# Optimization experiments

Measured on AMD Instinct MI355X. Metric: run time of the kernel, lower is better.

The kernel has to match this reference:

```python
import jax, jax.numpy as jnp
import numpy as np

B, N, DIM, K = 4, 4096, 128, 16


def setup_inputs() -> dict:
    key = jax.random.key(0)
    ks = jax.random.split(key, 20)
    s = 0.05
    inp = {
        "x": jax.random.normal(ks[0], (B, N, DIM), jnp.float32),
        "pos": jax.random.normal(ks[1], (B, N, 3), jnp.float32),
        # pos_mlp: Linear(3,dim) -> ReLU -> Linear(dim,dim)
        "pw1": jax.random.normal(ks[2], (3, DIM), jnp.float32) * s,
        "pb1": jnp.zeros((DIM,), jnp.float32),
        "pw2": jax.random.normal(ks[3], (DIM, DIM), jnp.float32) * s,
        "pb2": jnp.zeros((DIM,), jnp.float32),
        # q/k/v projections
        "qw": jax.random.normal(ks[4], (DIM, DIM), jnp.float32) * s,
        "qb": jnp.zeros((DIM,), jnp.float32),
        "kw": jax.random.normal(ks[5], (DIM, DIM), jnp.float32) * s,
        "kb": jnp.zeros((DIM,), jnp.float32),
        "vw": jax.random.normal(ks[6], (DIM, DIM), jnp.float32) * s,
        "vb": jnp.zeros((DIM,), jnp.float32),
        # attn MLP: Linear(dim, dim//4) -> ReLU -> Linear(dim//4, dim)
        "aw1": jax.random.normal(ks[7], (DIM, DIM // 4), jnp.float32) * s,
        "ab1": jnp.zeros((DIM // 4,), jnp.float32),
        "aw2": jax.random.normal(ks[8], (DIM // 4, DIM), jnp.float32) * s,
        "ab2": jnp.zeros((DIM,), jnp.float32),
    }
    return inp


def reference(x, pos, pw1, pb1, pw2, pb2, qw, qb, kw, kb, vw, vb, aw1, ab1, aw2, ab2):
    Bs, Np, C = x.shape
    k = K
    # pairwise squared distances: |pi|^2 + |pj|^2 - 2 pi.pj  -> (B,N,N)
    inner = jnp.einsum('bnd,bmd->bnm', pos, pos)
    xx = jnp.sum(pos * pos, axis=2, keepdims=True)  # (B,N,1)
    dist = xx + jnp.swapaxes(xx, 1, 2) - 2.0 * inner
    # k nearest neighbors (smallest dist) -> indices (B,N,k)
    _, idx = jax.lax.top_k(-dist, k)
    bidx = jnp.arange(Bs)[:, None, None]
    neighbors = x[bidx, idx]        # (B,N,k,C)
    pos_neighbors = pos[bidx, idx]  # (B,N,k,3)
    pos_relative = pos[:, :, None, :] - pos_neighbors  # (B,N,k,3)
    # pos MLP
    pe = jax.nn.relu(pos_relative @ pw1 + pb1) @ pw2 + pb2  # (B,N,k,C)
    q = (x @ qw + qb)[:, :, None, :]   # (B,N,1,C)
    kk = neighbors @ kw + kb           # (B,N,k,C)
    v = neighbors @ vw + vb            # (B,N,k,C)
    a = q - kk + pe
    attn = jax.nn.relu(a @ aw1 + ab1) @ aw2 + ab2  # (B,N,k,C)
    attn = jax.nn.softmax(attn, axis=2)
    out = jnp.sum(attn * (v + pe), axis=2)  # (B,N,C)
    return out
```

## Files before the change

### kernel.cpp

```cpp
#include <hip/hip_runtime.h>
#include <hip/hip_bf16.h>
#include <stdint.h>

#define BATCH 4
#define NPTS  4096
#define DIM   128
#define KNN   16
#define NROWS (BATCH*NPTS)
#define NCHUNK 16
#define CHUNK  (NPTS/NCHUNK)

typedef unsigned long long u64;
typedef unsigned int u32;
typedef unsigned short u16;
typedef __attribute__((ext_vector_type(8))) short short8;
typedef __attribute__((ext_vector_type(4))) float f32x4;

__device__ __forceinline__ u16 f2bf(float f) {
  u32 u = __float_as_uint(f);
  u += 0x7FFFu + ((u >> 16) & 1);
  return (u16)(u >> 16);
}

__global__ __launch_bounds__(256) void prep_pos4(const float* __restrict__ pos,
                                                 float4* __restrict__ pos4) {
  int i = blockIdx.x * 256 + threadIdx.x;
  if (i < NROWS) pos4[i] = make_float4(pos[3*i], pos[3*i+1], pos[3*i+2], 0.f);
}

__global__ __launch_bounds__(256) void prep_matmul(
    const float* __restrict__ pw2, const float* __restrict__ qw, const float* __restrict__ kw,
    const float* __restrict__ aw1,
    u16* __restrict__ w1T, float* __restrict__ Wq2, float* __restrict__ Wk2) {
  int p = blockIdx.x >> 2, qtr = blockIdx.x & 3;
  const float* A = p == 0 ? pw2 : (p == 1 ? qw : kw);
  int j = threadIdx.x & 31;
  int r0 = qtr*32 + (threadIdx.x >> 5)*4;
  float acc[4] = {0.f,0.f,0.f,0.f};
  for (int c = 0; c < 128; ++c) {
    float av = aw1[c*32 + j];
#pragma unroll
    for (int rr = 0; rr < 4; ++rr) acc[rr] = fmaf(A[(r0+rr)*128 + c], av, acc[rr]);
  }
#pragma unroll
  for (int rr = 0; rr < 4; ++rr) {
    int h = r0 + rr;
    if (p == 0)      w1T[j*128 + (h ^ ((j&7)<<3))] = f2bf(acc[rr]);
    else if (p == 1) Wq2[h*32 + j] = acc[rr];
    else             Wk2[h*32 + j] = acc[rr];
  }
}

__global__ __launch_bounds__(256) void prep_convert(
    const float* __restrict__ pw2, const float* __restrict__ aw2,
    const float* __restrict__ pw1, const float* __restrict__ pb1,
    const float* __restrict__ qb, const float* __restrict__ kb,
    const float* __restrict__ pb2, const float* __restrict__ aw1, const float* __restrict__ ab1,
    u16* __restrict__ pw2T, u16* __restrict__ aw2T,
    float4* __restrict__ pw1q, float* __restrict__ bias1) {
  int bid = blockIdx.x, tid = threadIdx.x;
  if (bid < 64) {
    int e = bid*256 + tid; int k = e >> 7, n = e & 127;
    pw2T[n*128 + (k ^ ((n&7)<<3))] = f2bf(pw2[k*128 + n]);
  } else if (bid < 80) {
    int e = (bid-64)*256 + tid; int k = e >> 7, n = e & 127;
    aw2T[n*32 + (k ^ ((n&3)<<3))] = f2bf(aw2[k*128 + n]);
  } else {
    if (tid < 128) {
      int c = tid;
      pw1q[c ^ ((c & 0x18) >> 2)] = make_float4(pw1[c], pw1[128+c], pw1[256+c], pb1[c]);
    } else if (tid < 160) {
      int j = tid - 128;
      float s = ab1[j];
      for (int c = 0; c < 128; ++c) s += (qb[c]-kb[c]+pb2[c]) * aw1[c*32+j];
      bias1[j] = s;
    }
  }
}

template <typename T>
__device__ __forceinline__ void cex(T& a, T& b) {
  T mn = a < b ? a : b;
  T mx = a < b ? b : a;
  a = mn; b = mx;
}
template <typename T>
__device__ __forceinline__ void sort16(T x[16]) {
#pragma unroll
  for (int k = 2; k <= 16; k <<= 1)
#pragma unroll
    for (int j = k >> 1; j > 0; j >>= 1)
#pragma unroll
      for (int i = 0; i < 16; ++i) {
        int l = i ^ j;
        if (l > i) { if ((i & k) == 0) cex(x[i], x[l]); else cex(x[l], x[i]); }
      }
}
template <typename T>
__device__ __forceinline__ void merge16(T A[16], const T B[16]) {
#pragma unroll
  for (int i = 0; i < 16; ++i) { T b = B[15 - i]; A[i] = A[i] < b ? A[i] : b; }
#pragma unroll
  for (int j = 8; j > 0; j >>= 1)
#pragma unroll
    for (int i = 0; i < 16; ++i) { int l = i ^ j; if (l > i) cex(A[i], A[l]); }
}
__device__ __forceinline__ void bmerge32(u32 x[32]) {
#pragma unroll
  for (int j = 16; j > 0; j >>= 1)
#pragma unroll
    for (int i = 0; i < 32; ++i) { int l = i ^ j; if (l > i) cex(x[i], x[l]); }
}

__global__ __launch_bounds__(256) void knn_scan(const float4* __restrict__ pos4,
                                                u32* __restrict__ part) {
  __shared__ float4 cs[4][CHUNK];
  const int lane  = threadIdx.x & 63;
  const int w     = threadIdx.x >> 6;
  const int task  = blockIdx.x * 4 + w;
  const int qg    = task >> 4;
  const int chunk = task & 15;
  const int qbase = qg * 64;
  const int b     = qbase >> 12;
  const int cbase = chunk * CHUNK;

  const float4* cand = pos4 + b*NPTS + cbase;
#pragma unroll
  for (int i = 0; i < CHUNK/64; ++i) cs[w][lane + 64*i] = cand[lane + 64*i];
  __syncthreads();

  float4 qp = pos4[qbase + lane];
  const float qx = qp.x, qy = qp.y, qz = qp.z;

  u32 best[16];
#pragma unroll
  for (int i = 0; i < 16; ++i) best[i] = ~0u;

#pragma unroll 1
  for (int m = 0; m < CHUNK/16; ++m) {
    u32 batch[16];
#pragma unroll
    for (int e = 0; e < 16; ++e) {
      float4 p = cs[w][m*16 + e];
      float dx = qx - p.x, dy = qy - p.y, dz = qz - p.z;
      float d  = fmaf(dx, dx, fmaf(dy, dy, dz*dz));
      batch[e] = (__float_as_uint(d) & 0xFFFFF000u) | (u32)(cbase + m*16 + e);
    }
    sort16(batch);
    merge16(best, batch);
  }
  const int q = qbase + lane;
  uint4* dst = (uint4*)(part + q*256 + chunk*16);
#pragma unroll
  for (int t = 0; t < 4; ++t)
    dst[t] = make_uint4(best[4*t], best[4*t+1], best[4*t+2], best[4*t+3]);
}

__global__ __launch_bounds__(256) void knn_refine(const float4* __restrict__ pos4,
                                                  const u32* __restrict__ part,
                                                  int* __restrict__ knnIdx) {
  __shared__ u64 A64[16][137];
  __shared__ u32 Bu[16][264];
  u32 (*Au)[274] = (u32 (*)[274])A64;

  const int tid = threadIdx.x;
  const int qi = tid >> 4, c = tid & 15;
  const int q  = blockIdx.x * 16 + qi;
  const int b  = q >> 12;

  {
    const uint4* src = (const uint4*)(part + q*256 + c*16);
    u32 own[16];
#pragma unroll
    for (int t = 0; t < 4; ++t) {
      uint4 v = src[t];
      own[4*t+0]=v.x; own[4*t+1]=v.y; own[4*t+2]=v.z; own[4*t+3]=v.w;
    }
#pragma unroll
    for (int s = 0; s < 16; ++s) Au[qi][c*17 + s] = own[s];
  }
  __syncthreads();

  if (c < 8) {
    u32 x[32];
#pragma unroll
    for (int s = 0; s < 16; ++s) x[s]      = Au[qi][(2*c)*17 + s];
#pragma unroll
    for (int s = 0; s < 16; ++s) x[16 + s] = Au[qi][(2*c+1)*17 + 15 - s];
    bmerge32(x);
#pragma unroll
    for (int s = 0; s < 32; ++s) Bu[qi][c*33 + s] = x[s];
  }
  __syncthreads();

  if (c < 4) {
    u32 x[32];
#pragma unroll
    for (int s = 0; s < 32; ++s) {
      u32 a = Bu[qi][(2*c)*33 + s], bb = Bu[qi][(2*c+1)*33 + 31 - s];
      x[s] = a < bb ? a : bb;
    }
    bmerge32(x);
#pragma unroll
    for (int s = 0; s < 32; ++s) Au[qi][c*33 + s] = x[s];
  }
  __syncthreads();

  if (c < 2) {
    u32 x[32];
#pragma unroll
    for (int s = 0; s < 32; ++s) {
      u32 a = Au[qi][(2*c)*33 + s], bb = Au[qi][(2*c+1)*33 + 31 - s];
      x[s] = a < bb ? a : bb;
    }
    bmerge32(x);
#pragma unroll
    for (int s = 0; s < 32; ++s) Bu[qi][c*33 + s] = x[s];
  }
  __syncthreads();

  if (c == 0) {
    u32 x[32];
#pragma unroll
    for (int s = 0; s < 32; ++s) {
      u32 a = Bu[qi][s], bb = Bu[qi][33 + 31 - s];
      x[s] = a < bb ? a : bb;
    }
    bmerge32(x);
#pragma unroll
    for (int s = 0; s < 32; ++s) Bu[qi][132 + s] = x[s];
  }
  __syncthreads();

  if (c < 2) {
    float4 qp = pos4[q];
    const double qx = qp.x, qy = qp.y, qz = qp.z;
    u64 key[16];
#pragma unroll
    for (int s = 0; s < 16; ++s) {
      int idx = (int)(Bu[qi][132 + c*16 + s] & 0xFFFu);
      float4 p = pos4[(b<<12) + idx];
      double dx = qx - (double)p.x;
      double dy = qy - (double)p.y;
      double dz = qz - (double)p.z;
      double d  = fma(dx, dx, fma(dy, dy, dz*dz));
      key[s] = (((u64)__double_as_longlong(d)) & ~0xFFFull) | (u64)idx;
    }
    sort16(key);
#pragma unroll
    for (int s = 0; s < 16; ++s) A64[qi][c*17 + s] = key[s];
  }
  __syncthreads();

  if (c == 0) {
    u64 best[16], nb[16];
#pragma unroll
    for (int s = 0; s < 16; ++s) { best[s] = A64[qi][s]; nb[s] = A64[qi][17 + s]; }
    merge16(best, nb);
    const int outq = q * KNN;
#pragma unroll
    for (int s = 0; s < 16; ++s) knnIdx[outq + s] = (int)(best[s] & 0xFFFull);
  }
}

__global__ __launch_bounds__(256) void proj_v(
    const float* __restrict__ x,
    const float* __restrict__ vw, const float* __restrict__ vb,
    const float* __restrict__ Wq2, const float* __restrict__ Wk2,
    float* __restrict__ vo, float* __restrict__ qa, float* __restrict__ ka) {
  __shared__ float xs[32*DIM];
  const int row0 = blockIdx.x * 32;
  const int tid = threadIdx.x;
  {
    const float4* src = (const float4*)(x + row0*DIM);
    float4* dst = (float4*)xs;
#pragma unroll
    for (int i = 0; i < 4; ++i) dst[tid + 256*i] = src[tid + 256*i];
  }
  __syncthreads();
  {
    const int c = tid & 127, g2 = tid >> 7;
    float av[16];
#pragma unroll
    for (int r = 0; r < 16; ++r) av[r] = 0.f;
    for (int d4 = 0; d4 < 32; ++d4) {
      float wv[4];
#pragma unroll
      for (int t = 0; t < 4; ++t) wv[t] = vw[(d4*4+t)*DIM + c];
#pragma unroll
      for (int r = 0; r < 16; ++r) {
        float4 xv = *(const float4*)&xs[(g2*16+r)*DIM + d4*4];
        av[r] = fmaf(xv.x, wv[0], av[r]);
        av[r] = fmaf(xv.y, wv[1], av[r]);
        av[r] = fmaf(xv.z, wv[2], av[r]);
        av[r] = fmaf(xv.w, wv[3], av[r]);
      }
    }
    float bv = vb[c];
#pragma unroll
    for (int r = 0; r < 16; ++r) vo[(row0 + g2*16 + r)*DIM + c] = av[r] + bv;
  }
  {
    const int j = tid & 31, grp = tid >> 5;
    float aq[4] = {0.f,0.f,0.f,0.f}, ak[4] = {0.f,0.f,0.f,0.f};
    for (int d4 = 0; d4 < 32; ++d4) {
#pragma unroll
      for (int t = 0; t < 4; ++t) {
        int d = d4*4 + t;
        float wq = Wq2[d*32 + j], wk = Wk2[d*32 + j];
#pragma unroll
        for (int rr = 0; rr < 4; ++rr) {
          float xv = xs[(grp*4+rr)*DIM + d];
          aq[rr] = fmaf(xv, wq, aq[rr]);
          ak[rr] = fmaf(xv, wk, ak[rr]);
        }
      }
    }
#pragma unroll
    for (int rr = 0; rr < 4; ++rr) {
      qa[(row0 + grp*4 + rr)*32 + j] = aq[rr];
      ka[(row0 + grp*4 + rr)*32 + j] = ak[rr];
    }
  }
}

__global__ __launch_bounds__(256) void attn_mfma(
    const float4* __restrict__ pos4, const int* __restrict__ knnIdx,
    const float* __restrict__ vws, const float* __restrict__ qa, const float* __restrict__ ka,
    const u16* __restrict__ pw2T, const u16* __restrict__ w1T, const u16* __restrict__ aw2T,
    const float4* __restrict__ pw1q, const float* __restrict__ bias1,
    const float* __restrict__ pb2, const float* __restrict__ ab2,
    float* __restrict__ out) {
  __shared__ __align__(16) u16 pw2s[16384];
  __shared__ __align__(16) u16 w1s[4096];
  __shared__ __align__(16) u16 aw2s[4096];
  __shared__ __align__(16) float4 pw1s[128];
  __shared__ float bias1s[32];
  __shared__ float pb2s[128];
  __shared__ float ab2s[128];
  __shared__ __align__(16) u16 h2t[4][512];
  __shared__ float4 rels[4][16];
  __shared__ int ids[4][16];

  const int tid = threadIdx.x;
  {
    const uint4* s1 = (const uint4*)pw2T; uint4* d1 = (uint4*)pw2s;
#pragma unroll
    for (int i = 0; i < 8; ++i) d1[tid + 256*i] = s1[tid + 256*i];
    const uint4* s2 = (const uint4*)w1T; uint4* d2 = (uint4*)w1s;
#pragma unroll
    for (int i = 0; i < 2; ++i) d2[tid + 256*i] = s2[tid + 256*i];
    const uint4* s3 = (const uint4*)aw2T; uint4* d3 = (uint4*)aw2s;
#pragma unroll
    for (int i = 0; i < 2; ++i) d3[tid + 256*i] = s3[tid + 256*i];
    if (tid < 128) { pw1s[tid] = pw1q[tid]; pb2s[tid] = pb2[tid]; ab2s[tid] = ab2[tid]; }
    else if (tid < 160) bias1s[tid-128] = bias1[tid-128];
  }
  __syncthreads();

  const int lane = tid & 63, w = tid >> 6;
  const int c16 = lane & 15, g = lane >> 4;

  for (int it = 0; it < 4; ++it) {
    const int q = blockIdx.x*16 + w*4 + it;
    const int b = q >> 12;
    if (lane < 16) {
      int id = knnIdx[q*KNN + lane];
      ids[w][lane] = id;
      float4 pq = pos4[q], pn = pos4[(b<<12) + id];
      rels[w][lane] = make_float4(pq.x-pn.x, pq.y-pn.y, pq.z-pn.z, 0.f);
    }
    __syncthreads();

    int idr[4];
#pragma unroll
    for (int r = 0; r < 4; ++r) idr[r] = ids[w][g*4 + r];

    float qa_v[2], ka_v[2][4];
#pragma unroll
    for (int t = 0; t < 2; ++t) qa_v[t] = qa[q*32 + t*16 + c16];
#pragma unroll
    for (int r = 0; r < 4; ++r)
#pragma unroll
      for (int t = 0; t < 2; ++t) ka_v[t][r] = ka[((b<<12)+idr[r])*32 + t*16 + c16];

    float4 rl = rels[w][c16];
    short8 h1f[4];
#pragma unroll
    for (int kc = 0; kc < 4; ++kc) {
      short8 s;
#pragma unroll
      for (int j = 0; j < 8; ++j) {
        int c = kc*32 + g*8 + j;
        float4 wv = pw1s[c ^ ((c & 0x18) >> 2)];
        float h = fmaf(rl.x, wv.x, fmaf(rl.y, wv.y, fmaf(rl.z, wv.z, wv.w)));
        s[j] = (short)f2bf(fmaxf(h, 0.f));
      }
      h1f[kc] = s;
    }

    f32x4 pe[8];
#pragma unroll
    for (int nt = 0; nt < 8; ++nt) { f32x4 z = {0.f,0.f,0.f,0.f}; pe[nt] = z; }
#pragma unroll
    for (int kc = 0; kc < 4; ++kc)
#pragma unroll
      for (int nt = 0; nt < 8; ++nt) {
        int n = nt*16 + c16;
        short8 bf = *(const short8*)&pw2s[n*128 + ((kc*32 + g*8) ^ ((n&7)<<3))];
        pe[nt] = __builtin_amdgcn_mfma_f32_16x16x32_bf16(h1f[kc], bf, pe[nt], 0, 0, 0);
      }

    f32x4 ha[2];
#pragma unroll
    for (int t = 0; t < 2; ++t) { f32x4 z = {0.f,0.f,0.f,0.f}; ha[t] = z; }
#pragma unroll
    for (int kc = 0; kc < 4; ++kc)
#pragma unroll
      for (int t = 0; t < 2; ++t) {
        int n = t*16 + c16;
        short8 bf = *(const short8*)&w1s[n*128 + ((kc*32 + g*8) ^ ((n&7)<<3))];
        ha[t] = __builtin_amdgcn_mfma_f32_16x16x32_bf16(h1f[kc], bf, ha[t], 0, 0, 0);
      }

#pragma unroll
    for (int t = 0; t < 2; ++t)
#pragma unroll
      for (int r = 0; r < 4; ++r) {
        float v = ha[t][r] + qa_v[t] - ka_v[t][r] + bias1s[t*16 + c16];
        int row = g*4 + r, col = t*16 + c16;
        h2t[w][row*32 + (col ^ ((row&3)<<3))] = f2bf(fmaxf(v, 0.f));
      }
    __syncthreads();

    short8 h2f = *(const short8*)&h2t[w][c16*32 + ((g*8) ^ ((c16&3)<<3))];

    f32x4 lg[8];
#pragma unroll
    for (int nt = 0; nt < 8; ++nt) {
      int n = nt*16 + c16;
      float ab = ab2s[n];
      f32x4 cini = {ab, ab, ab, ab};
      short8 bf = *(const short8*)&aw2s[n*32 + ((g*8) ^ ((n&3)<<3))];
      lg[nt] = __builtin_amdgcn_mfma_f32_16x16x32_bf16(h2f, bf, cini, 0, 0, 0);
    }

    float vv[8][4];
#pragma unroll
    for (int r = 0; r < 4; ++r) {
      const float* vrow = vws + (size_t)((b<<12) + idr[r])*DIM;
#pragma unroll
      for (int nt = 0; nt < 8; ++nt) vv[nt][r] = vrow[nt*16 + c16];
    }

#pragma unroll
    for (int nt = 0; nt < 8; ++nt) {
      float m = fmaxf(fmaxf(lg[nt][0], lg[nt][1]), fmaxf(lg[nt][2], lg[nt][3]));
      m = fmaxf(m, __shfl_xor(m, 16));
      m = fmaxf(m, __shfl_xor(m, 32));
      float e0 = __expf(lg[nt][0]-m), e1 = __expf(lg[nt][1]-m),
            e2 = __expf(lg[nt][2]-m), e3 = __expf(lg[nt][3]-m);
      float s = e0+e1+e2+e3;
      s += __shfl_xor(s, 16);
      s += __shfl_xor(s, 32);
      float inv = 1.0f / s;
      float pb = pb2s[nt*16 + c16];
      float acc = e0*(vv[nt][0] + pe[nt][0] + pb)
                + e1*(vv[nt][1] + pe[nt][1] + pb)
                + e2*(vv[nt][2] + pe[nt][2] + pb)
                + e3*(vv[nt][3] + pe[nt][3] + pb);
      acc *= inv;
      acc += __shfl_xor(acc, 16);
      acc += __shfl_xor(acc, 32);
      if (lane < 16) out[q*DIM + nt*16 + lane] = acc;
    }
  }
}

extern "C" void kernel_launch(void* const* d_in, const int* in_sizes, int n_in,
                              void* d_out, int out_size, void* d_ws, size_t ws_size,
                              hipStream_t stream) {
  const float* x   = (const float*)d_in[0];
  const float* pos = (const float*)d_in[1];
  const float* pw1 = (const float*)d_in[2];
  const float* pb1 = (const float*)d_in[3];
  const float* pw2 = (const float*)d_in[4];
  const float* pb2 = (const float*)d_in[5];
  const float* qw  = (const float*)d_in[6];
  const float* qb  = (const float*)d_in[7];
  const float* kw  = (const float*)d_in[8];
  const float* kb  = (const float*)d_in[9];
  const float* vw  = (const float*)d_in[10];
  const float* vb  = (const float*)d_in[11];
  const float* aw1 = (const float*)d_in[12];
  const float* ab1 = (const float*)d_in[13];
  const float* aw2 = (const float*)d_in[14];
  const float* ab2 = (const float*)d_in[15];
  float* out = (float*)d_out;

  char* ws = (char*)d_ws;
  float4* pos4   = (float4*)(ws);
  int*    knnIdx = (int*)(ws + (1u<<20));
  u32*    part   = (u32*)(ws + (2u<<20));
  float*  vws    = (float*)(ws + (2u<<20));
  float*  qa     = (float*)(ws + (11u<<20));
  float*  ka     = (float*)(ws + (13u<<20));
  char*   wsw    = ws + (19u<<20);
  u16*    pw2T  = (u16*)(wsw);
  u16*    w1T   = (u16*)(wsw + 32768);
  u16*    aw2T  = (u16*)(wsw + 40960);
  float4* pw1q  = (float4*)(wsw + 49152);
  float*  bias1 = (float*)(wsw + 51200);
  float*  Wq2   = (float*)(wsw + 51328);
  float*  Wk2   = (float*)(wsw + 67712);

  prep_pos4<<<NROWS/256, 256, 0, stream>>>(pos, pos4);
  prep_matmul<<<12, 256, 0, stream>>>(pw2, qw, kw, aw1, w1T, Wq2, Wk2);
  prep_convert<<<81, 256, 0, stream>>>(pw2, aw2, pw1, pb1, qb, kb, pb2, aw1, ab1,
                                       pw2T, aw2T, pw1q, bias1);
  knn_scan<<<(NROWS/64)*NCHUNK/4, 256, 0, stream>>>(pos4, part);
  knn_refine<<<NROWS/16, 256, 0, stream>>>(pos4, part, knnIdx);
  proj_v<<<NROWS/32, 256, 0, stream>>>(x, vw, vb, Wq2, Wk2, vws, qa, ka);
  attn_mfma<<<NROWS/16, 256, 0, stream>>>(pos4, knnIdx, vws, qa, ka,
                                          pw2T, w1T, aw2T, pw1q, bias1, pb2, ab2, out);
}
```

Before: 251.8 us.

## Merge prep kernels, MFMA projections, kNN early-skip, register-resident attn weights

Folds the three prep kernels into one launch and adds bf16 transposed copies of vw, Wq2 and Wk2. The fp32 scalar projection kernel becomes a bf16 MFMA kernel. knn_scan skips the sort and merge of a batch when no lane has a candidate that beats its current worst neighbor. attn_mfma keeps the w1 and aw2 fragments in registers, exchanges neighbor ids and relative positions with shuffles instead of shared memory, replaces block barriers with a wave-level LDS wait, and swizzles block order. The projections lose precision through the bf16 conversion, and register pressure in the attention kernel rises.

```diff
diff --git a/kernel.cpp b/kernel.cpp
--- a/kernel.cpp
+++ b/kernel.cpp
@@ -22,50 +22,32 @@
   return (u16)(u >> 16);
 }
 
-__global__ __launch_bounds__(256) void prep_pos4(const float* __restrict__ pos,
-                                                 float4* __restrict__ pos4) {
-  int i = blockIdx.x * 256 + threadIdx.x;
-  if (i < NROWS) pos4[i] = make_float4(pos[3*i], pos[3*i+1], pos[3*i+2], 0.f);
-}
-
-__global__ __launch_bounds__(256) void prep_matmul(
-    const float* __restrict__ pw2, const float* __restrict__ qw, const float* __restrict__ kw,
-    const float* __restrict__ aw1,
-    u16* __restrict__ w1T, float* __restrict__ Wq2, float* __restrict__ Wk2) {
-  int p = blockIdx.x >> 2, qtr = blockIdx.x & 3;
-  const float* A = p == 0 ? pw2 : (p == 1 ? qw : kw);
-  int j = threadIdx.x & 31;
-  int r0 = qtr*32 + (threadIdx.x >> 5)*4;
-  float acc[4] = {0.f,0.f,0.f,0.f};
-  for (int c = 0; c < 128; ++c) {
-    float av = aw1[c*32 + j];
-#pragma unroll
-    for (int rr = 0; rr < 4; ++rr) acc[rr] = fmaf(A[(r0+rr)*128 + c], av, acc[rr]);
-  }
-#pragma unroll
-  for (int rr = 0; rr < 4; ++rr) {
-    int h = r0 + rr;
-    if (p == 0)      w1T[j*128 + (h ^ ((j&7)<<3))] = f2bf(acc[rr]);
-    else if (p == 1) Wq2[h*32 + j] = acc[rr];
-    else             Wk2[h*32 + j] = acc[rr];
-  }
-}
-
-__global__ __launch_bounds__(256) void prep_convert(
-    const float* __restrict__ pw2, const float* __restrict__ aw2,
+#define WAVE_LDS_FENCE() asm volatile("s_waitcnt lgkmcnt(0)" ::: "memory")
+
+__global__ __launch_bounds__(256) void prep_all(
+    const float* __restrict__ pos,
     const float* __restrict__ pw1, const float* __restrict__ pb1,
-    const float* __restrict__ qb, const float* __restrict__ kb,
-    const float* __restrict__ pb2, const float* __restrict__ aw1, const float* __restrict__ ab1,
-    u16* __restrict__ pw2T, u16* __restrict__ aw2T,
+    const float* __restrict__ pw2, const float* __restrict__ pb2,
+    const float* __restrict__ qw, const float* __restrict__ qb,
+    const float* __restrict__ kw, const float* __restrict__ kb,
+    const float* __restrict__ vw,
+    const float* __restrict__ aw1, const float* __restrict__ ab1,
+    const float* __restrict__ aw2,
+    float4* __restrict__ pos4, u16* __restrict__ pw2T, u16* __restrict__ aw2T,
+    u16* __restrict__ vwT, u16* __restrict__ w1T,
+    u16* __restrict__ Wq2T, u16* __restrict__ Wk2T,
     float4* __restrict__ pw1q, float* __restrict__ bias1) {
-  int bid = blockIdx.x, tid = threadIdx.x;
+  const int bid = blockIdx.x, tid = threadIdx.x;
   if (bid < 64) {
-    int e = bid*256 + tid; int k = e >> 7, n = e & 127;
+    int e = bid*256 + tid, k = e >> 7, n = e & 127;
     pw2T[n*128 + (k ^ ((n&7)<<3))] = f2bf(pw2[k*128 + n]);
   } else if (bid < 80) {
-    int e = (bid-64)*256 + tid; int k = e >> 7, n = e & 127;
+    int e = (bid-64)*256 + tid, k = e >> 7, n = e & 127;
     aw2T[n*32 + (k ^ ((n&3)<<3))] = f2bf(aw2[k*128 + n]);
-  } else {
+  } else if (bid < 144) {
+    int e = (bid-80)*256 + tid, k = e >> 7, n = e & 127;
+    vwT[n*128 + (k ^ ((n&7)<<3))] = f2bf(vw[k*128 + n]);
+  } else if (bid == 144) {
     if (tid < 128) {
       int c = tid;
       pw1q[c ^ ((c & 0x18) >> 2)] = make_float4(pw1[c], pw1[128+c], pw1[256+c], pb1[c]);
@@ -75,6 +57,27 @@
       for (int c = 0; c < 128; ++c) s += (qb[c]-kb[c]+pb2[c]) * aw1[c*32+j];
       bias1[j] = s;
     }
+  } else if (bid < 157) {
+    int p = (bid-145) >> 2, qtr = (bid-145) & 3;
+    const float* A = p == 0 ? pw2 : (p == 1 ? qw : kw);
+    int j = tid & 31, r0 = qtr*32 + (tid >> 5)*4;
+    float acc[4] = {0.f,0.f,0.f,0.f};
+    for (int c = 0; c < 128; ++c) {
+      float av = aw1[c*32 + j];
+#pragma unroll
+      for (int rr = 0; rr < 4; ++rr) acc[rr] = fmaf(A[(r0+rr)*128 + c], av, acc[rr]);
+    }
+#pragma unroll
+    for (int rr = 0; rr < 4; ++rr) {
+      int h = r0 + rr;
+      u16 v = f2bf(acc[rr]);
+      if (p == 0)      w1T [j*128 + (h ^ ((j&7)<<3))] = v;
+      else if (p == 1) Wq2T[j*128 + (h ^ ((j&7)<<3))] = v;
+      else             Wk2T[j*128 + (h ^ ((j&7)<<3))] = v;
+    }
+  } else {
+    int i = (bid-157)*256 + tid;
+    if (i < NROWS) pos4[i] = make_float4(pos[3*i], pos[3*i+1], pos[3*i+2], 0.f);
   }
 }
 
@@ -146,8 +149,13 @@
       float d  = fmaf(dx, dx, fmaf(dy, dy, dz*dz));
       batch[e] = (__float_as_uint(d) & 0xFFFFF000u) | (u32)(cbase + m*16 + e);
     }
-    sort16(batch);
-    merge16(best, batch);
+    u32 bmin = batch[0];
+#pragma unroll
+    for (int e = 1; e < 16; ++e) bmin = batch[e] < bmin ? batch[e] : bmin;
+    if (__any(bmin < best[15])) {
+      sort16(batch);
+      merge16(best, batch);
+    }
   }
   const int q = qbase + lane;
   uint4* dst = (uint4*)(part + q*256 + chunk*16);
@@ -263,68 +271,62 @@
   }
 }
 
-__global__ __launch_bounds__(256) void proj_v(
-    const float* __restrict__ x,
-    const float* __restrict__ vw, const float* __restrict__ vb,
-    const float* __restrict__ Wq2, const float* __restrict__ Wk2,
+__global__ __launch_bounds__(256) void proj_mfma(
+    const float* __restrict__ x, const u16* __restrict__ vwT,
+    const u16* __restrict__ Wq2T, const u16* __restrict__ Wk2T,
+    const float* __restrict__ vb,
     float* __restrict__ vo, float* __restrict__ qa, float* __restrict__ ka) {
-  __shared__ float xs[32*DIM];
-  const int row0 = blockIdx.x * 32;
-  const int tid = threadIdx.x;
-  {
-    const float4* src = (const float4*)(x + row0*DIM);
-    float4* dst = (float4*)xs;
-#pragma unroll
-    for (int i = 0; i < 4; ++i) dst[tid + 256*i] = src[tid + 256*i];
-  }
-  __syncthreads();
-  {
-    const int c = tid & 127, g2 = tid >> 7;
-    float av[16];
-#pragma unroll
-    for (int r = 0; r < 16; ++r) av[r] = 0.f;
-    for (int d4 = 0; d4 < 32; ++d4) {
-      float wv[4];
-#pragma unroll
-      for (int t = 0; t < 4; ++t) wv[t] = vw[(d4*4+t)*DIM + c];
-#pragma unroll
-      for (int r = 0; r < 16; ++r) {
-        float4 xv = *(const float4*)&xs[(g2*16+r)*DIM + d4*4];
-        av[r] = fmaf(xv.x, wv[0], av[r]);
-        av[r] = fmaf(xv.y, wv[1], av[r]);
-        av[r] = fmaf(xv.z, wv[2], av[r]);
-        av[r] = fmaf(xv.w, wv[3], av[r]);
-      }
-    }
-    float bv = vb[c];
-#pragma unroll
-    for (int r = 0; r < 16; ++r) vo[(row0 + g2*16 + r)*DIM + c] = av[r] + bv;
-  }
-  {
-    const int j = tid & 31, grp = tid >> 5;
-    float aq[4] = {0.f,0.f,0.f,0.f}, ak[4] = {0.f,0.f,0.f,0.f};
-    for (int d4 = 0; d4 < 32; ++d4) {
-#pragma unroll
-      for (int t = 0; t < 4; ++t) {
-        int d = d4*4 + t;
-        float wq = Wq2[d*32 + j], wk = Wk2[d*32 + j];
-#pragma unroll
-        for (int rr = 0; rr < 4; ++rr) {
-          float xv = xs[(grp*4+rr)*DIM + d];
-          aq[rr] = fmaf(xv, wq, aq[rr]);
-          ak[rr] = fmaf(xv, wk, ak[rr]);
-        }
-      }
-    }
-#pragma unroll
-    for (int rr = 0; rr < 4; ++rr) {
-      qa[(row0 + grp*4 + rr)*32 + j] = aq[rr];
-      ka[(row0 + grp*4 + rr)*32 + j] = ak[rr];
-    }
-  }
-}
-
-__global__ __launch_bounds__(256) void attn_mfma(
+  const int lane = threadIdx.x & 63, w = threadIdx.x >> 6;
+  const int c16 = lane & 15, g = lane >> 4;
+  const int row0 = (blockIdx.x*4 + w)*16;
+
+  const float* xrow = x + (size_t)(row0 + c16)*DIM;
+  short8 af[4];
+#pragma unroll
+  for (int kc = 0; kc < 4; ++kc) {
+    float4 a0 = *(const float4*)&xrow[kc*32 + g*8];
+    float4 a1 = *(const float4*)&xrow[kc*32 + g*8 + 4];
+    short8 s;
+    s[0]=(short)f2bf(a0.x); s[1]=(short)f2bf(a0.y); s[2]=(short)f2bf(a0.z); s[3]=(short)f2bf(a0.w);
+    s[4]=(short)f2bf(a1.x); s[5]=(short)f2bf(a1.y); s[6]=(short)f2bf(a1.z); s[7]=(short)f2bf(a1.w);
+    af[kc] = s;
+  }
+
+#pragma unroll
+  for (int nt = 0; nt < 8; ++nt) {
+    int n = nt*16 + c16;
+    float bb = vb[n];
+    f32x4 acc = {bb, bb, bb, bb};
+#pragma unroll
+    for (int kc = 0; kc < 4; ++kc) {
+      short8 bf = *(const short8*)&vwT[n*128 + ((kc*32 + g*8) ^ ((n&7)<<3))];
+      acc = __builtin_amdgcn_mfma_f32_16x16x32_bf16(af[kc], bf, acc, 0, 0, 0);
+    }
+#pragma unroll
+    for (int r = 0; r < 4; ++r)
+      vo[(size_t)(row0 + g*4 + r)*DIM + n] = acc[r];
+  }
+
+#pragma unroll
+  for (int t = 0; t < 2; ++t) {
+    int n = t*16 + c16;
+    f32x4 aq = {0.f,0.f,0.f,0.f}, ak = {0.f,0.f,0.f,0.f};
+#pragma unroll
+    for (int kc = 0; kc < 4; ++kc) {
+      short8 bq = *(const short8*)&Wq2T[n*128 + ((kc*32 + g*8) ^ ((n&7)<<3))];
+      short8 bk = *(const short8*)&Wk2T[n*128 + ((kc*32 + g*8) ^ ((n&7)<<3))];
+      aq = __builtin_amdgcn_mfma_f32_16x16x32_bf16(af[kc], bq, aq, 0, 0, 0);
+      ak = __builtin_amdgcn_mfma_f32_16x16x32_bf16(af[kc], bk, ak, 0, 0, 0);
+    }
+#pragma unroll
+    for (int r = 0; r < 4; ++r) {
+      qa[(row0 + g*4 + r)*32 + n] = aq[r];
+      ka[(row0 + g*4 + r)*32 + n] = ak[r];
+    }
+  }
+}
+
+__global__ __launch_bounds__(256, 4) void attn_mfma(
     const float4* __restrict__ pos4, const int* __restrict__ knnIdx,
     const float* __restrict__ vws, const float* __restrict__ qa, const float* __restrict__ ka,
     const u16* __restrict__ pw2T, const u16* __restrict__ w1T, const u16* __restrict__ aw2T,
@@ -332,27 +334,15 @@
     const float* __restrict__ pb2, const float* __restrict__ ab2,
     float* __restrict__ out) {
   __shared__ __align__(16) u16 pw2s[16384];
-  __shared__ __align__(16) u16 w1s[4096];
-  __shared__ __align__(16) u16 aw2s[4096];
   __shared__ __align__(16) float4 pw1s[128];
-  __shared__ float bias1s[32];
-  __shared__ float pb2s[128];
-  __shared__ float ab2s[128];
+  __shared__ float bias1s[32], pb2s[128], ab2s[128];
   __shared__ __align__(16) u16 h2t[4][512];
-  __shared__ float4 rels[4][16];
-  __shared__ int ids[4][16];
 
   const int tid = threadIdx.x;
   {
     const uint4* s1 = (const uint4*)pw2T; uint4* d1 = (uint4*)pw2s;
 #pragma unroll
     for (int i = 0; i < 8; ++i) d1[tid + 256*i] = s1[tid + 256*i];
-    const uint4* s2 = (const uint4*)w1T; uint4* d2 = (uint4*)w1s;
-#pragma unroll
-    for (int i = 0; i < 2; ++i) d2[tid + 256*i] = s2[tid + 256*i];
-    const uint4* s3 = (const uint4*)aw2T; uint4* d3 = (uint4*)aw2s;
-#pragma unroll
-    for (int i = 0; i < 2; ++i) d3[tid + 256*i] = s3[tid + 256*i];
     if (tid < 128) { pw1s[tid] = pw1q[tid]; pb2s[tid] = pb2[tid]; ab2s[tid] = ab2[tid]; }
     else if (tid < 160) bias1s[tid-128] = bias1[tid-128];
   }
@@ -361,20 +351,40 @@
   const int lane = tid & 63, w = tid >> 6;
   const int c16 = lane & 15, g = lane >> 4;
 
-  for (int it = 0; it < 4; ++it) {
-    const int q = blockIdx.x*16 + w*4 + it;
-    const int b = q >> 12;
-    if (lane < 16) {
-      int id = knnIdx[q*KNN + lane];
-      ids[w][lane] = id;
-      float4 pq = pos4[q], pn = pos4[(b<<12) + id];
-      rels[w][lane] = make_float4(pq.x-pn.x, pq.y-pn.y, pq.z-pn.z, 0.f);
-    }
-    __syncthreads();
-
+  short8 Bw1[4][2];
+#pragma unroll
+  for (int kc = 0; kc < 4; ++kc)
+#pragma unroll
+    for (int t = 0; t < 2; ++t) {
+      int n = t*16 + c16;
+      Bw1[kc][t] = *(const short8*)&w1T[n*128 + ((kc*32 + g*8) ^ ((n&7)<<3))];
+    }
+  short8 Baw2[8];
+#pragma unroll
+  for (int nt = 0; nt < 8; ++nt) {
+    int n = nt*16 + c16;
+    Baw2[nt] = *(const short8*)&aw2T[n*32 + ((g*8) ^ ((n&3)<<3))];
+  }
+
+  const int swz = (blockIdx.x & 7) * 128 + (blockIdx.x >> 3);
+  const int qblock = swz * 16;
+  const int qbase  = qblock + w * 4;
+  const int bofs   = (qblock >> 12) << 12;
+
+  int id_own = knnIdx[qbase*KNN + lane];
+  float4 pq = pos4[qbase + g];
+  float4 pn = pos4[bofs + id_own];
+  float rox = pq.x - pn.x, roy = pq.y - pn.y, roz = pq.z - pn.z;
+
+#pragma unroll
+  for (int j = 0; j < 4; ++j) {
+    const int q = qbase + j;
+    float relx = __shfl(rox, j*16 + c16);
+    float rely = __shfl(roy, j*16 + c16);
+    float relz = __shfl(roz, j*16 + c16);
     int idr[4];
 #pragma unroll
-    for (int r = 0; r < 4; ++r) idr[r] = ids[w][g*4 + r];
+    for (int r = 0; r < 4; ++r) idr[r] = __shfl(id_own, j*16 + g*4 + r);
 
     float qa_v[2], ka_v[2][4];
 #pragma unroll
@@ -382,19 +392,18 @@
 #pragma unroll
     for (int r = 0; r < 4; ++r)
 #pragma unroll
-      for (int t = 0; t < 2; ++t) ka_v[t][r] = ka[((b<<12)+idr[r])*32 + t*16 + c16];
-
-    float4 rl = rels[w][c16];
+      for (int t = 0; t < 2; ++t) ka_v[t][r] = ka[(bofs + idr[r])*32 + t*16 + c16];
+
     short8 h1f[4];
 #pragma unroll
     for (int kc = 0; kc < 4; ++kc) {
       short8 s;
 #pragma unroll
-      for (int j = 0; j < 8; ++j) {
-        int c = kc*32 + g*8 + j;
+      for (int jj = 0; jj < 8; ++jj) {
+        int c = kc*32 + g*8 + jj;
         float4 wv = pw1s[c ^ ((c & 0x18) >> 2)];
-        float h = fmaf(rl.x, wv.x, fmaf(rl.y, wv.y, fmaf(rl.z, wv.z, wv.w)));
-        s[j] = (short)f2bf(fmaxf(h, 0.f));
+        float h = fmaf(relx, wv.x, fmaf(rely, wv.y, fmaf(relz, wv.z, wv.w)));
+        s[jj] = (short)f2bf(fmaxf(h, 0.f));
       }
       h1f[kc] = s;
     }
@@ -417,11 +426,8 @@
 #pragma unroll
     for (int kc = 0; kc < 4; ++kc)
 #pragma unroll
-      for (int t = 0; t < 2; ++t) {
-        int n = t*16 + c16;
-        short8 bf = *(const short8*)&w1s[n*128 + ((kc*32 + g*8) ^ ((n&7)<<3))];
-        ha[t] = __builtin_amdgcn_mfma_f32_16x16x32_bf16(h1f[kc], bf, ha[t], 0, 0, 0);
-      }
+      for (int t = 0; t < 2; ++t)
+        ha[t] = __builtin_amdgcn_mfma_f32_16x16x32_bf16(h1f[kc], Bw1[kc][t], ha[t], 0, 0, 0);
 
 #pragma unroll
     for (int t = 0; t < 2; ++t)
@@ -431,26 +437,16 @@
         int row = g*4 + r, col = t*16 + c16;
         h2t[w][row*32 + (col ^ ((row&3)<<3))] = f2bf(fmaxf(v, 0.f));
       }
-    __syncthreads();
+    WAVE_LDS_FENCE();
 
     short8 h2f = *(const short8*)&h2t[w][c16*32 + ((g*8) ^ ((c16&3)<<3))];
 
     f32x4 lg[8];
 #pragma unroll
     for (int nt = 0; nt < 8; ++nt) {
-      int n = nt*16 + c16;
-      float ab = ab2s[n];
+      float ab = ab2s[nt*16 + c16];
       f32x4 cini = {ab, ab, ab, ab};
-      short8 bf = *(const short8*)&aw2s[n*32 + ((g*8) ^ ((n&3)<<3))];
-      lg[nt] = __builtin_amdgcn_mfma_f32_16x16x32_bf16(h2f, bf, cini, 0, 0, 0);
-    }
-
-    float vv[8][4];
-#pragma unroll
-    for (int r = 0; r < 4; ++r) {
-      const float* vrow = vws + (size_t)((b<<12) + idr[r])*DIM;
-#pragma unroll
-      for (int nt = 0; nt < 8; ++nt) vv[nt][r] = vrow[nt*16 + c16];
+      lg[nt] = __builtin_amdgcn_mfma_f32_16x16x32_bf16(h2f, Baw2[nt], cini, 0, 0, 0);
     }
 
 #pragma unroll
@@ -465,10 +461,14 @@
       s += __shfl_xor(s, 32);
       float inv = 1.0f / s;
       float pb = pb2s[nt*16 + c16];
-      float acc = e0*(vv[nt][0] + pe[nt][0] + pb)
-                + e1*(vv[nt][1] + pe[nt][1] + pb)
-                + e2*(vv[nt][2] + pe[nt][2] + pb)
-                + e3*(vv[nt][3] + pe[nt][3] + pb);
+      float v0 = vws[(size_t)(bofs + idr[0])*DIM + nt*16 + c16];
+      float v1 = vws[(size_t)(bofs + idr[1])*DIM + nt*16 + c16];
+      float v2 = vws[(size_t)(bofs + idr[2])*DIM + nt*16 + c16];
+      float v3 = vws[(size_t)(bofs + idr[3])*DIM + nt*16 + c16];
+      float acc = e0*(v0 + pe[nt][0] + pb)
+                + e1*(v1 + pe[nt][1] + pb)
+                + e2*(v2 + pe[nt][2] + pb)
+                + e3*(v3 + pe[nt][3] + pb);
       acc *= inv;
       acc += __shfl_xor(acc, 16);
       acc += __shfl_xor(acc, 32);
@@ -509,18 +509,18 @@
   u16*    pw2T  = (u16*)(wsw);
   u16*    w1T   = (u16*)(wsw + 32768);
   u16*    aw2T  = (u16*)(wsw + 40960);
-  float4* pw1q  = (float4*)(wsw + 49152);
-  float*  bias1 = (float*)(wsw + 51200);
-  float*  Wq2   = (float*)(wsw + 51328);
-  float*  Wk2   = (float*)(wsw + 67712);
-
-  prep_pos4<<<NROWS/256, 256, 0, stream>>>(pos, pos4);
-  prep_matmul<<<12, 256, 0, stream>>>(pw2, qw, kw, aw1, w1T, Wq2, Wk2);
-  prep_convert<<<81, 256, 0, stream>>>(pw2, aw2, pw1, pb1, qb, kb, pb2, aw1, ab1,
-                                       pw2T, aw2T, pw1q, bias1);
+  u16*    vwT   = (u16*)(wsw + 49152);
+  u16*    Wq2T  = (u16*)(wsw + 81920);
+  u16*    Wk2T  = (u16*)(wsw + 90112);
+  float4* pw1q  = (float4*)(wsw + 98304);
+  float*  bias1 = (float*)(wsw + 100352);
+
+  prep_all<<<221, 256, 0, stream>>>(pos, pw1, pb1, pw2, pb2, qw, qb, kw, kb, vw,
+                                    aw1, ab1, aw2,
+                                    pos4, pw2T, aw2T, vwT, w1T, Wq2T, Wk2T, pw1q, bias1);
   knn_scan<<<(NROWS/64)*NCHUNK/4, 256, 0, stream>>>(pos4, part);
   knn_refine<<<NROWS/16, 256, 0, stream>>>(pos4, part, knnIdx);
-  proj_v<<<NROWS/32, 256, 0, stream>>>(x, vw, vb, Wq2, Wk2, vws, qa, ka);
+  proj_mfma<<<NROWS/64, 256, 0, stream>>>(x, vwT, Wq2T, Wk2T, vb, vws, qa, ka);
   attn_mfma<<<NROWS/16, 256, 0, stream>>>(pos4, knnIdx, vws, qa, ka,
                                           pw2T, w1T, aw2T, pw1q, bias1, pb2, ab2, out);
 }
```

Result: slower. 261.3 us (+3.8%).
